# Optimization experiments

Measured on AMD Instinct MI355X. Metric: run time of the kernel, lower is better.

Reference implementation:

```python
import jax, jax.numpy as jnp
import numpy as np
import math

B, S, D, H = 4, 2048, 1024, 16
HD = D // H  # 64
SCALE = math.sqrt(HD)  # scale=True -> sqrt(d_model // n_head)

def setup_inputs() -> dict:
    key = jax.random.key(0)
    k1, k2, k3, k4, k5 = jax.random.split(key, 5)
    x = jax.random.normal(k1, (B, S, D), dtype=jnp.float32)
    char_ids = jax.random.randint(k2, (B, S), 0, 21128)
    seq_len = jax.random.randint(k3, (B,), 1, S)
    mask = jnp.ones((B, S), dtype=jnp.int64)
    W_qkv = jax.random.normal(k4, (D, 3 * D), dtype=jnp.float32) * (1.0 / math.sqrt(D))
    W_fc = jax.random.normal(k5, (D, D), dtype=jnp.float32) * (1.0 / math.sqrt(D))
    b_fc = jnp.zeros((D,), dtype=jnp.float32)
    return {"x": x, "char_ids": char_ids, "seq_len": seq_len, "mask": mask,
            "W_qkv": W_qkv, "W_fc": W_fc, "b_fc": b_fc}

def reference(x, char_ids, seq_len, mask, W_qkv, W_fc, b_fc):
    b, s, d = x.shape
    qkv = x @ W_qkv                      # [b, s, 3d]
    q, k, v = jnp.split(qkv, 3, axis=-1)
    # [b, h, s, hd]
    q = q.reshape(b, s, H, HD).transpose(0, 2, 1, 3)
    k = k.reshape(b, s, H, HD).transpose(0, 2, 1, 3)
    v = v.reshape(b, s, H, HD).transpose(0, 2, 1, 3)
    attn = jnp.einsum('bhqd,bhkd->bhqk', q, k) / SCALE
    attn = jnp.where(mask[:, None, None, :] == 0, -jnp.inf, attn)
    attn = jax.nn.softmax(attn, axis=-1)
    # dropout is identity in eval mode
    out = jnp.einsum('bhqk,bhkd->bhqd', attn, v)
    out = out.transpose(0, 2, 1, 3).reshape(b, s, d)
    return out @ W_fc + b_fc
```

## Files before the change

kernel.cpp:

```cpp
#include <hip/hip_runtime.h>
#include <hip/hip_bf16.h>


#define S_ 2048
#define D_ 1024

typedef __attribute__((ext_vector_type(4))) float f32x4;
typedef __attribute__((ext_vector_type(16))) float f32x16;
typedef __attribute__((ext_vector_type(8))) short bf16x8;

__device__ __forceinline__ unsigned short f2b(float f) {
  union { float f; unsigned u; } x; x.f = f;
  unsigned r = x.u + 0x7fffu + ((x.u >> 16) & 1u);
  return (unsigned short)(r >> 16);
}
__device__ __forceinline__ float b2f(unsigned short u) {
  union { unsigned u; float f; } x; x.u = ((unsigned)u) << 16; return x.f;
}

__device__ __forceinline__ void gload_lds16(const void* g, void* l) {
  __builtin_amdgcn_global_load_lds(
      (const __attribute__((address_space(1))) unsigned int*)g,
      (__attribute__((address_space(3))) unsigned int*)l, 16, 0, 0);
}

__global__ void cvt_f32_bf16(const float* __restrict__ in, unsigned short* __restrict__ out, int n) {
  int i = (blockIdx.x * blockDim.x + threadIdx.x) * 8;
  if (i >= n) return;
  float4 a = *(const float4*)&in[i];
  float4 b = *(const float4*)&in[i + 4];
  unsigned short r[8];
  r[0] = f2b(a.x); r[1] = f2b(a.y); r[2] = f2b(a.z); r[3] = f2b(a.w);
  r[4] = f2b(b.x); r[5] = f2b(b.y); r[6] = f2b(b.z); r[7] = f2b(b.w);
  *(uint4*)&out[i] = *(uint4*)r;
}

__global__ void transpose_cvt(const float* __restrict__ W, unsigned short* __restrict__ Wt,
                              int K, int N) {
  __shared__ unsigned short tile[32][33];
  int n0 = blockIdx.x * 32, k0 = blockIdx.y * 32;
  int tx = threadIdx.x & 31, ty = threadIdx.x >> 5;
  #pragma unroll
  for (int i = 0; i < 32; i += 8)
    tile[ty + i][tx] = f2b(W[(size_t)(k0 + ty + i) * N + n0 + tx]);
  __syncthreads();
  #pragma unroll
  for (int i = 0; i < 32; i += 8)
    Wt[(size_t)(n0 + ty + i) * K + k0 + tx] = tile[tx][ty + i];
}

__global__ __launch_bounds__(256) void gemm_bt(const unsigned short* __restrict__ A,
                                               const unsigned short* __restrict__ Bt,
                                               const float* __restrict__ bias,
                                               float* __restrict__ Cf,
                                               unsigned short* __restrict__ Cb,
                                               int M, int N, int K) {
  __shared__ unsigned short As[128 * 32];
  __shared__ unsigned short Bs[128 * 32];
  int tid = threadIdx.x, wave = tid >> 6, lane = tid & 63;
  int bm = blockIdx.x, bn = blockIdx.y;
  int wr = (wave >> 1) * 64, wc = (wave & 1) * 64;
  f32x4 acc[4][4] = {};

  const unsigned short* aG0 = A + (size_t)(bm * 128 + wave * 32 + (lane >> 2)) * K + (lane & 3) * 8;
  const unsigned short* aG1 = aG0 + (size_t)16 * K;
  const unsigned short* bG0 = Bt + (size_t)(bn * 128 + wave * 32 + (lane >> 2)) * K + (lane & 3) * 8;
  const unsigned short* bG1 = bG0 + (size_t)16 * K;
  unsigned short* aL0 = As + wave * 32 * 32;
  unsigned short* aL1 = aL0 + 16 * 32;
  unsigned short* bL0 = Bs + wave * 32 * 32;
  unsigned short* bL1 = bL0 + 16 * 32;

  for (int k0 = 0; k0 < K; k0 += 32) {
    gload_lds16(aG0, aL0); gload_lds16(aG1, aL1);
    gload_lds16(bG0, bL0); gload_lds16(bG1, bL1);
    aG0 += 32; aG1 += 32; bG0 += 32; bG1 += 32;
    __syncthreads();
    bf16x8 af[4], bf[4];
    #pragma unroll
    for (int i = 0; i < 4; i++)
      af[i] = *(const bf16x8*)&As[(wr + i * 16 + (lane & 15)) * 32 + (lane >> 4) * 8];
    #pragma unroll
    for (int i = 0; i < 4; i++)
      bf[i] = *(const bf16x8*)&Bs[(wc + i * 16 + (lane & 15)) * 32 + (lane >> 4) * 8];
    #pragma unroll
    for (int i = 0; i < 4; i++)
      #pragma unroll
      for (int j = 0; j < 4; j++)
        acc[i][j] = __builtin_amdgcn_mfma_f32_16x16x32_bf16(af[i], bf[j], acc[i][j], 0, 0, 0);
    __syncthreads();
  }

  int row0 = bm * 128 + wr + (lane >> 4) * 4;
  int col0 = bn * 128 + wc + (lane & 15);
  if (Cb) {
    #pragma unroll
    for (int i = 0; i < 4; i++)
      #pragma unroll
      for (int j = 0; j < 4; j++)
        #pragma unroll
        for (int q = 0; q < 4; q++)
          Cb[(size_t)(row0 + i * 16 + q) * N + col0 + j * 16] = f2b(acc[i][j][q]);
  } else {
    #pragma unroll
    for (int i = 0; i < 4; i++)
      #pragma unroll
      for (int j = 0; j < 4; j++) {
        float bv = bias[col0 + j * 16];
        #pragma unroll
        for (int q = 0; q < 4; q++)
          Cf[(size_t)(row0 + i * 16 + q) * N + col0 + j * 16] = acc[i][j][q] + bv;
      }
  }
}

__global__ __launch_bounds__(256) void flash_attn(const unsigned short* __restrict__ qkv,
                                                  unsigned short* __restrict__ ao) {
  __shared__ unsigned short Ks[2][4096];
  __shared__ unsigned short Vs[2][4096];
  int tid = threadIdx.x, wave = tid >> 6, lane = tid & 63;
  int l31 = lane & 31, hi = lane >> 5;
  int bh = blockIdx.x, b = bh >> 4, h = bh & 15;
  const unsigned short* base = qkv + (size_t)b * S_ * 3072 + h * 64;
  const unsigned short* kb = base + 1024;
  const unsigned short* vb = base + 2048;
  int q0 = blockIdx.y * 128 + wave * 32;

  bf16x8 qf[4];
  {
    const unsigned short* qp = base + (size_t)(q0 + l31) * 3072 + hi * 8;
    #pragma unroll
    for (int ks = 0; ks < 4; ks++) {
      bf16x8 v = *(const bf16x8*)(qp + ks * 16);
      #pragma unroll
      for (int e = 0; e < 8; e++) v[e] = (short)f2b(0.125f * b2f((unsigned short)v[e]));
      qf[ks] = v;
    }
  }

  f32x16 o0a = {}, o0b = {}, o1a = {}, o1b = {};
  float mi = -1e30f, li = 0.f;

  int r_l = lane >> 3;
  int gsrc = (lane & 7) ^ r_l;
  size_t koffA = (size_t)((wave * 2 + 0) * 8 + r_l) * 3072 + gsrc * 8;
  size_t koffB = (size_t)((wave * 2 + 1) * 8 + r_l) * 3072 + gsrc * 8;
  int kvv = tid & 63, dgr = (tid >> 6) * 16;
  bf16x8 vr0, vr1;

  {
    gload_lds16(kb + koffA, &Ks[0][(wave * 2 + 0) * 512]);
    gload_lds16(kb + koffB, &Ks[0][(wave * 2 + 1) * 512]);
    const unsigned short* vsrc = vb + (size_t)kvv * 3072 + dgr;
    vr0 = *(const bf16x8*)vsrc;
    vr1 = *(const bf16x8*)(vsrc + 8);
    #pragma unroll
    for (int e = 0; e < 16; e++) {
      int d = dgr + e;
      Vs[0][d * 64 + ((((kvv >> 3) ^ (d & 7)) << 3)) + (kvv & 7)] =
          (unsigned short)(e < 8 ? vr0[e] : vr1[e - 8]);
    }
    __syncthreads();
  }

  for (int t = 0; t < 32; ++t) {
    int cur = t & 1;
    int tn = (t + 1) & 31;
    {
      const unsigned short* ksrc = kb + (size_t)tn * 64 * 3072;
      gload_lds16(ksrc + koffA, &Ks[cur ^ 1][(wave * 2 + 0) * 512]);
      gload_lds16(ksrc + koffB, &Ks[cur ^ 1][(wave * 2 + 1) * 512]);
      const unsigned short* vsrc = vb + (size_t)(tn * 64 + kvv) * 3072 + dgr;
      vr0 = *(const bf16x8*)vsrc;
      vr1 = *(const bf16x8*)(vsrc + 8);
    }

    const unsigned short* Kc = Ks[cur];
    const unsigned short* Vc = Vs[cur];

    #pragma unroll
    for (int sub = 0; sub < 2; ++sub) {
      f32x16 sA = {};
      __builtin_amdgcn_s_setprio(1);
      #pragma unroll
      for (int ks = 0; ks < 4; ks++) {
        int row = sub * 32 + l31;
        bf16x8 kf = *(const bf16x8*)&Kc[row * 64 + ((((ks << 1) + hi) ^ (row & 7)) << 3)];
        sA = __builtin_amdgcn_mfma_f32_32x32x16_bf16(kf, qf[ks], sA, 0, 0, 0);
      }
      __builtin_amdgcn_s_setprio(0);

      float t0 = fmaxf(fmaxf(sA[0], sA[1]), sA[2]);
      float t1 = fmaxf(fmaxf(sA[3], sA[4]), sA[5]);
      float t2 = fmaxf(fmaxf(sA[6], sA[7]), sA[8]);
      float t3 = fmaxf(fmaxf(sA[9], sA[10]), sA[11]);
      float t4 = fmaxf(fmaxf(sA[12], sA[13]), sA[14]);
      float tm = fmaxf(fmaxf(fmaxf(t0, t1), t2), fmaxf(fmaxf(t3, t4), sA[15]));
      tm = fmaxf(tm, __shfl_xor(tm, 32, 64));
      if (__any(tm > mi + 8.f)) {
        float tnew = fmaxf(mi, tm);
        float fac = __expf(mi - tnew);
        li *= fac; mi = tnew;
        #pragma unroll
        for (int r = 0; r < 16; r++) {
          o0a[r] *= fac; o0b[r] *= fac; o1a[r] *= fac; o1b[r] *= fac;
        }
      }
      float p[16];
      float rs = 0.f;
      #pragma unroll
      for (int r = 0; r < 16; r++) { p[r] = __expf(sA[r] - mi); rs += p[r]; }
      li += rs;

      unsigned c0, c1, c2, c3, c4, c5, c6, c7;
      asm("v_cvt_pk_bf16_f32 %0, %1, %2" : "=v"(c0) : "v"(p[0]),  "v"(p[1]));
      asm("v_cvt_pk_bf16_f32 %0, %1, %2" : "=v"(c1) : "v"(p[2]),  "v"(p[3]));
      asm("v_cvt_pk_bf16_f32 %0, %1, %2" : "=v"(c2) : "v"(p[4]),  "v"(p[5]));
      asm("v_cvt_pk_bf16_f32 %0, %1, %2" : "=v"(c3) : "v"(p[6]),  "v"(p[7]));
      asm("v_cvt_pk_bf16_f32 %0, %1, %2" : "=v"(c4) : "v"(p[8]),  "v"(p[9]));
      asm("v_cvt_pk_bf16_f32 %0, %1, %2" : "=v"(c5) : "v"(p[10]), "v"(p[11]));
      asm("v_cvt_pk_bf16_f32 %0, %1, %2" : "=v"(c6) : "v"(p[12]), "v"(p[13]));
      asm("v_cvt_pk_bf16_f32 %0, %1, %2" : "=v"(c7) : "v"(p[14]), "v"(p[15]));
      asm volatile("v_permlane32_swap_b32 %0, %1" : "+v"(c0), "+v"(c2));
      asm volatile("v_permlane32_swap_b32 %0, %1" : "+v"(c1), "+v"(c3));
      asm volatile("v_permlane32_swap_b32 %0, %1" : "+v"(c4), "+v"(c6));
      asm volatile("v_permlane32_swap_b32 %0, %1" : "+v"(c5), "+v"(c7));
      union { unsigned u[4]; bf16x8 v; } P0, P1;
      P0.u[0] = c0; P0.u[1] = c1; P0.u[2] = c2; P0.u[3] = c3;
      P1.u[0] = c4; P1.u[1] = c5; P1.u[2] = c6; P1.u[3] = c7;

      int slot0 = (sub << 2) + hi;
      int slot1 = (sub << 2) + 2 + hi;
      bf16x8 vA0 = *(const bf16x8*)&Vc[l31 * 64 + ((slot0 ^ (l31 & 7)) << 3)];
      bf16x8 vA1 = *(const bf16x8*)&Vc[(32 + l31) * 64 + ((slot0 ^ (l31 & 7)) << 3)];
      bf16x8 vB0 = *(const bf16x8*)&Vc[l31 * 64 + ((slot1 ^ (l31 & 7)) << 3)];
      bf16x8 vB1 = *(const bf16x8*)&Vc[(32 + l31) * 64 + ((slot1 ^ (l31 & 7)) << 3)];
      __builtin_amdgcn_s_setprio(1);
      o0a = __builtin_amdgcn_mfma_f32_32x32x16_bf16(vA0, P0.v, o0a, 0, 0, 0);
      o1a = __builtin_amdgcn_mfma_f32_32x32x16_bf16(vA1, P0.v, o1a, 0, 0, 0);
      o0b = __builtin_amdgcn_mfma_f32_32x32x16_bf16(vB0, P1.v, o0b, 0, 0, 0);
      o1b = __builtin_amdgcn_mfma_f32_32x32x16_bf16(vB1, P1.v, o1b, 0, 0, 0);
      __builtin_amdgcn_s_setprio(0);
    }

    {
      unsigned short* Vd = Vs[cur ^ 1];
      #pragma unroll
      for (int e = 0; e < 16; e++) {
        int d = dgr + e;
        Vd[d * 64 + ((((kvv >> 3) ^ (d & 7)) << 3)) + (kvv & 7)] =
            (unsigned short)(e < 8 ? vr0[e] : vr1[e - 8]);
      }
    }
    __syncthreads();
  }

  li += __shfl_xor(li, 32, 64);
  float inv = 1.f / li;
  unsigned short* aop = ao + (size_t)(b * S_ + q0 + l31) * D_ + h * 64;
  #pragma unroll
  for (int g = 0; g < 4; g++) {
    union { unsigned short s[4]; uint2 u; } w0, w1;
    #pragma unroll
    for (int e = 0; e < 4; e++) {
      w0.s[e] = f2b((o0a[g * 4 + e] + o0b[g * 4 + e]) * inv);
      w1.s[e] = f2b((o1a[g * 4 + e] + o1b[g * 4 + e]) * inv);
    }
    int d = g * 8 + hi * 4;
    *(uint2*)&aop[d] = w0.u;
    *(uint2*)&aop[32 + d] = w1.u;
  }
}

extern "C" void kernel_launch(void* const* d_in, const int* in_sizes, int n_in,
                              void* d_out, int out_size, void* d_ws, size_t ws_size,
                              hipStream_t stream) {
  const float* x    = (const float*)d_in[0];
  const float* Wqkv = (const float*)d_in[4];
  const float* Wfc  = (const float*)d_in[5];
  const float* bfc  = (const float*)d_in[6];
  float* out = (float*)d_out;

  char* ws = (char*)d_ws;
  unsigned short* xb    = (unsigned short*)(ws);
  unsigned short* qkv   = (unsigned short*)(ws + 16777216);
  unsigned short* ao    = (unsigned short*)(ws + 67108864);
  unsigned short* wqkvT = (unsigned short*)(ws + 83886080);
  unsigned short* wfcT  = (unsigned short*)(ws + 90177536);

  cvt_f32_bf16<<<dim3(4096), dim3(256), 0, stream>>>(x, xb, 8388608);
  transpose_cvt<<<dim3(96, 32), dim3(256), 0, stream>>>(Wqkv, wqkvT, 1024, 3072);
  transpose_cvt<<<dim3(32, 32), dim3(256), 0, stream>>>(Wfc, wfcT, 1024, 1024);
  gemm_bt<<<dim3(64, 24), dim3(256), 0, stream>>>(xb, wqkvT, nullptr, nullptr, qkv, 8192, 3072, 1024);
  flash_attn<<<dim3(64, 16), dim3(256), 0, stream>>>(qkv, ao);
  gemm_bt<<<dim3(64, 8), dim3(256), 0, stream>>>(ao, wfcT, bfc, out, nullptr, 8192, 1024, 1024);
}
```

Before: 237.3 us.

## Fuse x fp32-to-bf16 conversion into QKV GEMM and swizzle workgroup order

Removes the standalone kernel that converted x to bf16. The QKV GEMM now loads fp32 x directly, converts it in registers and writes the result to LDS, which saves one launch and a 16MB write plus re-read. It also remaps workgroup indices in groups of 8 to improve L2 reuse of B tiles. The trade-off is that the fp32 A loads are synchronous register loads instead of async global-to-LDS loads. Since A is re-read once per N-tile (24 times), the fp32 read traffic for A doubles inside the GEMM.

```diff
diff --git a/kernel.cpp b/kernel.cpp
--- a/kernel.cpp
+++ b/kernel.cpp
@@ -22,17 +22,6 @@
   __builtin_amdgcn_global_load_lds(
       (const __attribute__((address_space(1))) unsigned int*)g,
       (__attribute__((address_space(3))) unsigned int*)l, 16, 0, 0);
-}
-
-__global__ void cvt_f32_bf16(const float* __restrict__ in, unsigned short* __restrict__ out, int n) {
-  int i = (blockIdx.x * blockDim.x + threadIdx.x) * 8;
-  if (i >= n) return;
-  float4 a = *(const float4*)&in[i];
-  float4 b = *(const float4*)&in[i + 4];
-  unsigned short r[8];
-  r[0] = f2b(a.x); r[1] = f2b(a.y); r[2] = f2b(a.z); r[3] = f2b(a.w);
-  r[4] = f2b(b.x); r[5] = f2b(b.y); r[6] = f2b(b.z); r[7] = f2b(b.w);
-  *(uint4*)&out[i] = *(uint4*)r;
 }
 
 __global__ void transpose_cvt(const float* __restrict__ W, unsigned short* __restrict__ Wt,
@@ -49,7 +38,8 @@
     Wt[(size_t)(n0 + ty + i) * K + k0 + tx] = tile[tx][ty + i];
 }
 
-__global__ __launch_bounds__(256) void gemm_bt(const unsigned short* __restrict__ A,
+template <bool AF32>
+__global__ __launch_bounds__(256) void gemm_bt(const void* __restrict__ Av,
                                                const unsigned short* __restrict__ Bt,
                                                const float* __restrict__ bias,
                                                float* __restrict__ Cf,
@@ -58,23 +48,49 @@
   __shared__ unsigned short As[128 * 32];
   __shared__ unsigned short Bs[128 * 32];
   int tid = threadIdx.x, wave = tid >> 6, lane = tid & 63;
-  int bm = blockIdx.x, bn = blockIdx.y;
+
+  int lin = blockIdx.y * 64 + blockIdx.x;
+  int nwg = gridDim.y * 64;
+  int qq = nwg >> 3;
+  int swz = (lin & 7) * qq + (lin >> 3);
+  int bm = swz & 63, bn = swz >> 6;
+
   int wr = (wave >> 1) * 64, wc = (wave & 1) * 64;
   f32x4 acc[4][4] = {};
 
-  const unsigned short* aG0 = A + (size_t)(bm * 128 + wave * 32 + (lane >> 2)) * K + (lane & 3) * 8;
-  const unsigned short* aG1 = aG0 + (size_t)16 * K;
-  const unsigned short* bG0 = Bt + (size_t)(bn * 128 + wave * 32 + (lane >> 2)) * K + (lane & 3) * 8;
+  int arow = wave * 32 + (lane >> 2);
+  int acol = (lane & 3) * 8;
+  const unsigned short* bG0 = Bt + (size_t)(bn * 128 + wave * 32 + (lane >> 2)) * K + acol;
   const unsigned short* bG1 = bG0 + (size_t)16 * K;
-  unsigned short* aL0 = As + wave * 32 * 32;
-  unsigned short* aL1 = aL0 + 16 * 32;
   unsigned short* bL0 = Bs + wave * 32 * 32;
   unsigned short* bL1 = bL0 + 16 * 32;
+  unsigned short* aW = As + arow * 32 + acol;
+
+  const unsigned short* aB16 = nullptr;
+  const float* aF32 = nullptr;
+  if constexpr (AF32) aF32 = (const float*)Av + (size_t)(bm * 128 + arow) * K + acol;
+  else                aB16 = (const unsigned short*)Av + (size_t)(bm * 128 + arow) * K + acol;
 
   for (int k0 = 0; k0 < K; k0 += 32) {
-    gload_lds16(aG0, aL0); gload_lds16(aG1, aL1);
     gload_lds16(bG0, bL0); gload_lds16(bG1, bL1);
-    aG0 += 32; aG1 += 32; bG0 += 32; bG1 += 32;
+    bG0 += 32; bG1 += 32;
+    if constexpr (AF32) {
+      float4 a0 = *(const float4*)aF32;
+      float4 a1 = *(const float4*)(aF32 + 4);
+      float4 c0 = *(const float4*)(aF32 + (size_t)16 * K);
+      float4 c1 = *(const float4*)(aF32 + (size_t)16 * K + 4);
+      aF32 += 32;
+      unsigned short r[8], s[8];
+      r[0]=f2b(a0.x); r[1]=f2b(a0.y); r[2]=f2b(a0.z); r[3]=f2b(a0.w);
+      r[4]=f2b(a1.x); r[5]=f2b(a1.y); r[6]=f2b(a1.z); r[7]=f2b(a1.w);
+      s[0]=f2b(c0.x); s[1]=f2b(c0.y); s[2]=f2b(c0.z); s[3]=f2b(c0.w);
+      s[4]=f2b(c1.x); s[5]=f2b(c1.y); s[6]=f2b(c1.z); s[7]=f2b(c1.w);
+      *(uint4*)aW = *(uint4*)r;
+      *(uint4*)(aW + 16 * 32) = *(uint4*)s;
+    } else {
+      gload_lds16(aB16, aW); gload_lds16(aB16 + (size_t)16 * K, aW + 16 * 32);
+      aB16 += 32;
+    }
     __syncthreads();
     bf16x8 af[4], bf[4];
     #pragma unroll
@@ -282,16 +298,16 @@
   float* out = (float*)d_out;
 
   char* ws = (char*)d_ws;
-  unsigned short* xb    = (unsigned short*)(ws);
-  unsigned short* qkv   = (unsigned short*)(ws + 16777216);
-  unsigned short* ao    = (unsigned short*)(ws + 67108864);
-  unsigned short* wqkvT = (unsigned short*)(ws + 83886080);
-  unsigned short* wfcT  = (unsigned short*)(ws + 90177536);
-
-  cvt_f32_bf16<<<dim3(4096), dim3(256), 0, stream>>>(x, xb, 8388608);
+  unsigned short* qkv   = (unsigned short*)(ws);
+  unsigned short* ao    = (unsigned short*)(ws + 50331648);
+  unsigned short* wqkvT = (unsigned short*)(ws + 67108864);
+  unsigned short* wfcT  = (unsigned short*)(ws + 73400320);
+
   transpose_cvt<<<dim3(96, 32), dim3(256), 0, stream>>>(Wqkv, wqkvT, 1024, 3072);
   transpose_cvt<<<dim3(32, 32), dim3(256), 0, stream>>>(Wfc, wfcT, 1024, 1024);
-  gemm_bt<<<dim3(64, 24), dim3(256), 0, stream>>>(xb, wqkvT, nullptr, nullptr, qkv, 8192, 3072, 1024);
+  gemm_bt<true><<<dim3(64, 24), dim3(256), 0, stream>>>(x, wqkvT, nullptr, nullptr, qkv,
+                                                        8192, 3072, 1024);
   flash_attn<<<dim3(64, 16), dim3(256), 0, stream>>>(qkv, ao);
-  gemm_bt<<<dim3(64, 8), dim3(256), 0, stream>>>(ao, wfcT, bfc, out, nullptr, 8192, 1024, 1024);
-}
+  gemm_bt<false><<<dim3(64, 8), dim3(256), 0, stream>>>(ao, wfcT, bfc, out, nullptr,
+                                                        8192, 1024, 1024);
+}
```

New measurement: 270.8 us. 14.1% more time.

## Process two query tiles per wave in flash attention to reuse K/V tiles

Applied to the files above, without the earlier changes.

Each wave now handles two 32-row query blocks (A and B, 128 rows apart), so each block covers 256 queries and the grid halves along y. The K and V fragments read from LDS and the global K/V loads are shared by twice as many query rows, cutting LDS and global traffic per unit of compute and adding independent MFMA chains for latency hiding. The cost is roughly double the accumulator and softmax register use, which may lower occupancy, and only 512 blocks are launched, which lowers parallelism on a large GPU.

```diff
diff --git a/kernel.cpp b/kernel.cpp
--- a/kernel.cpp
+++ b/kernel.cpp
@@ -124,22 +124,27 @@
   const unsigned short* base = qkv + (size_t)b * S_ * 3072 + h * 64;
   const unsigned short* kb = base + 1024;
   const unsigned short* vb = base + 2048;
-  int q0 = blockIdx.y * 128 + wave * 32;
-
-  bf16x8 qf[4];
+  int q0 = blockIdx.y * 256 + wave * 32;
+
+  bf16x8 qfA[4], qfB[4];
   {
-    const unsigned short* qp = base + (size_t)(q0 + l31) * 3072 + hi * 8;
+    const unsigned short* qpA = base + (size_t)(q0 + l31) * 3072 + hi * 8;
+    const unsigned short* qpB = qpA + (size_t)128 * 3072;
     #pragma unroll
     for (int ks = 0; ks < 4; ks++) {
-      bf16x8 v = *(const bf16x8*)(qp + ks * 16);
-      #pragma unroll
-      for (int e = 0; e < 8; e++) v[e] = (short)f2b(0.125f * b2f((unsigned short)v[e]));
-      qf[ks] = v;
-    }
-  }
-
-  f32x16 o0a = {}, o0b = {}, o1a = {}, o1b = {};
-  float mi = -1e30f, li = 0.f;
+      bf16x8 va = *(const bf16x8*)(qpA + ks * 16);
+      bf16x8 vc = *(const bf16x8*)(qpB + ks * 16);
+      #pragma unroll
+      for (int e = 0; e < 8; e++) {
+        va[e] = (short)f2b(0.125f * b2f((unsigned short)va[e]));
+        vc[e] = (short)f2b(0.125f * b2f((unsigned short)vc[e]));
+      }
+      qfA[ks] = va; qfB[ks] = vc;
+    }
+  }
+
+  f32x16 oA0 = {}, oA1 = {}, oB0 = {}, oB1 = {};
+  float miA = -1e30f, liA = 0.f, miB = -1e30f, liB = 0.f;
 
   int r_l = lane >> 3;
   int gsrc = (lane & 7) ^ r_l;
@@ -180,66 +185,107 @@
 
     #pragma unroll
     for (int sub = 0; sub < 2; ++sub) {
-      f32x16 sA = {};
+      f32x16 sA = {}, sB = {};
       __builtin_amdgcn_s_setprio(1);
       #pragma unroll
       for (int ks = 0; ks < 4; ks++) {
         int row = sub * 32 + l31;
         bf16x8 kf = *(const bf16x8*)&Kc[row * 64 + ((((ks << 1) + hi) ^ (row & 7)) << 3)];
-        sA = __builtin_amdgcn_mfma_f32_32x32x16_bf16(kf, qf[ks], sA, 0, 0, 0);
+        sA = __builtin_amdgcn_mfma_f32_32x32x16_bf16(kf, qfA[ks], sA, 0, 0, 0);
+        sB = __builtin_amdgcn_mfma_f32_32x32x16_bf16(kf, qfB[ks], sB, 0, 0, 0);
       }
       __builtin_amdgcn_s_setprio(0);
 
-      float t0 = fmaxf(fmaxf(sA[0], sA[1]), sA[2]);
-      float t1 = fmaxf(fmaxf(sA[3], sA[4]), sA[5]);
-      float t2 = fmaxf(fmaxf(sA[6], sA[7]), sA[8]);
-      float t3 = fmaxf(fmaxf(sA[9], sA[10]), sA[11]);
-      float t4 = fmaxf(fmaxf(sA[12], sA[13]), sA[14]);
-      float tm = fmaxf(fmaxf(fmaxf(t0, t1), t2), fmaxf(fmaxf(t3, t4), sA[15]));
-      tm = fmaxf(tm, __shfl_xor(tm, 32, 64));
-      if (__any(tm > mi + 8.f)) {
-        float tnew = fmaxf(mi, tm);
-        float fac = __expf(mi - tnew);
-        li *= fac; mi = tnew;
+      union { unsigned u[4]; bf16x8 v; } PA0, PA1;
+      {
+        float t0 = fmaxf(fmaxf(sA[0], sA[1]), sA[2]);
+        float t1 = fmaxf(fmaxf(sA[3], sA[4]), sA[5]);
+        float t2 = fmaxf(fmaxf(sA[6], sA[7]), sA[8]);
+        float t3 = fmaxf(fmaxf(sA[9], sA[10]), sA[11]);
+        float t4 = fmaxf(fmaxf(sA[12], sA[13]), sA[14]);
+        float tm = fmaxf(fmaxf(fmaxf(t0, t1), t2), fmaxf(fmaxf(t3, t4), sA[15]));
+        tm = fmaxf(tm, __shfl_xor(tm, 32, 64));
+        if (__any(tm > miA + 8.f)) {
+          float tnew = fmaxf(miA, tm);
+          float fac = __expf(miA - tnew);
+          liA *= fac; miA = tnew;
+          #pragma unroll
+          for (int r = 0; r < 16; r++) { oA0[r] *= fac; oA1[r] *= fac; }
+        }
+        float p[16];
+        float rs = 0.f;
         #pragma unroll
-        for (int r = 0; r < 16; r++) {
-          o0a[r] *= fac; o0b[r] *= fac; o1a[r] *= fac; o1b[r] *= fac;
+        for (int r = 0; r < 16; r++) { p[r] = __expf(sA[r] - miA); rs += p[r]; }
+        liA += rs;
+        unsigned c0, c1, c2, c3, c4, c5, c6, c7;
+        asm("v_cvt_pk_bf16_f32 %0, %1, %2" : "=v"(c0) : "v"(p[0]),  "v"(p[1]));
+        asm("v_cvt_pk_bf16_f32 %0, %1, %2" : "=v"(c1) : "v"(p[2]),  "v"(p[3]));
+        asm("v_cvt_pk_bf16_f32 %0, %1, %2" : "=v"(c2) : "v"(p[4]),  "v"(p[5]));
+        asm("v_cvt_pk_bf16_f32 %0, %1, %2" : "=v"(c3) : "v"(p[6]),  "v"(p[7]));
+        asm("v_cvt_pk_bf16_f32 %0, %1, %2" : "=v"(c4) : "v"(p[8]),  "v"(p[9]));
+        asm("v_cvt_pk_bf16_f32 %0, %1, %2" : "=v"(c5) : "v"(p[10]), "v"(p[11]));
+        asm("v_cvt_pk_bf16_f32 %0, %1, %2" : "=v"(c6) : "v"(p[12]), "v"(p[13]));
+        asm("v_cvt_pk_bf16_f32 %0, %1, %2" : "=v"(c7) : "v"(p[14]), "v"(p[15]));
+        asm volatile("v_permlane32_swap_b32 %0, %1" : "+v"(c0), "+v"(c2));
+        asm volatile("v_permlane32_swap_b32 %0, %1" : "+v"(c1), "+v"(c3));
+        asm volatile("v_permlane32_swap_b32 %0, %1" : "+v"(c4), "+v"(c6));
+        asm volatile("v_permlane32_swap_b32 %0, %1" : "+v"(c5), "+v"(c7));
+        PA0.u[0] = c0; PA0.u[1] = c1; PA0.u[2] = c2; PA0.u[3] = c3;
+        PA1.u[0] = c4; PA1.u[1] = c5; PA1.u[2] = c6; PA1.u[3] = c7;
+      }
+      union { unsigned u[4]; bf16x8 v; } PB0, PB1;
+      {
+        float t0 = fmaxf(fmaxf(sB[0], sB[1]), sB[2]);
+        float t1 = fmaxf(fmaxf(sB[3], sB[4]), sB[5]);
+        float t2 = fmaxf(fmaxf(sB[6], sB[7]), sB[8]);
+        float t3 = fmaxf(fmaxf(sB[9], sB[10]), sB[11]);
+        float t4 = fmaxf(fmaxf(sB[12], sB[13]), sB[14]);
+        float tm = fmaxf(fmaxf(fmaxf(t0, t1), t2), fmaxf(fmaxf(t3, t4), sB[15]));
+        tm = fmaxf(tm, __shfl_xor(tm, 32, 64));
+        if (__any(tm > miB + 8.f)) {
+          float tnew = fmaxf(miB, tm);
+          float fac = __expf(miB - tnew);
+          liB *= fac; miB = tnew;
+          #pragma unroll
+          for (int r = 0; r < 16; r++) { oB0[r] *= fac; oB1[r] *= fac; }
         }
-      }
-      float p[16];
-      float rs = 0.f;
-      #pragma unroll
-      for (int r = 0; r < 16; r++) { p[r] = __expf(sA[r] - mi); rs += p[r]; }
-      li += rs;
-
-      unsigned c0, c1, c2, c3, c4, c5, c6, c7;
-      asm("v_cvt_pk_bf16_f32 %0, %1, %2" : "=v"(c0) : "v"(p[0]),  "v"(p[1]));
-      asm("v_cvt_pk_bf16_f32 %0, %1, %2" : "=v"(c1) : "v"(p[2]),  "v"(p[3]));
-      asm("v_cvt_pk_bf16_f32 %0, %1, %2" : "=v"(c2) : "v"(p[4]),  "v"(p[5]));
-      asm("v_cvt_pk_bf16_f32 %0, %1, %2" : "=v"(c3) : "v"(p[6]),  "v"(p[7]));
-      asm("v_cvt_pk_bf16_f32 %0, %1, %2" : "=v"(c4) : "v"(p[8]),  "v"(p[9]));
-      asm("v_cvt_pk_bf16_f32 %0, %1, %2" : "=v"(c5) : "v"(p[10]), "v"(p[11]));
-      asm("v_cvt_pk_bf16_f32 %0, %1, %2" : "=v"(c6) : "v"(p[12]), "v"(p[13]));
-      asm("v_cvt_pk_bf16_f32 %0, %1, %2" : "=v"(c7) : "v"(p[14]), "v"(p[15]));
-      asm volatile("v_permlane32_swap_b32 %0, %1" : "+v"(c0), "+v"(c2));
-      asm volatile("v_permlane32_swap_b32 %0, %1" : "+v"(c1), "+v"(c3));
-      asm volatile("v_permlane32_swap_b32 %0, %1" : "+v"(c4), "+v"(c6));
-      asm volatile("v_permlane32_swap_b32 %0, %1" : "+v"(c5), "+v"(c7));
-      union { unsigned u[4]; bf16x8 v; } P0, P1;
-      P0.u[0] = c0; P0.u[1] = c1; P0.u[2] = c2; P0.u[3] = c3;
-      P1.u[0] = c4; P1.u[1] = c5; P1.u[2] = c6; P1.u[3] = c7;
+        float p[16];
+        float rs = 0.f;
+        #pragma unroll
+        for (int r = 0; r < 16; r++) { p[r] = __expf(sB[r] - miB); rs += p[r]; }
+        liB += rs;
+        unsigned c0, c1, c2, c3, c4, c5, c6, c7;
+        asm("v_cvt_pk_bf16_f32 %0, %1, %2" : "=v"(c0) : "v"(p[0]),  "v"(p[1]));
+        asm("v_cvt_pk_bf16_f32 %0, %1, %2" : "=v"(c1) : "v"(p[2]),  "v"(p[3]));
+        asm("v_cvt_pk_bf16_f32 %0, %1, %2" : "=v"(c2) : "v"(p[4]),  "v"(p[5]));
+        asm("v_cvt_pk_bf16_f32 %0, %1, %2" : "=v"(c3) : "v"(p[6]),  "v"(p[7]));
+        asm("v_cvt_pk_bf16_f32 %0, %1, %2" : "=v"(c4) : "v"(p[8]),  "v"(p[9]));
+        asm("v_cvt_pk_bf16_f32 %0, %1, %2" : "=v"(c5) : "v"(p[10]), "v"(p[11]));
+        asm("v_cvt_pk_bf16_f32 %0, %1, %2" : "=v"(c6) : "v"(p[12]), "v"(p[13]));
+        asm("v_cvt_pk_bf16_f32 %0, %1, %2" : "=v"(c7) : "v"(p[14]), "v"(p[15]));
+        asm volatile("v_permlane32_swap_b32 %0, %1" : "+v"(c0), "+v"(c2));
+        asm volatile("v_permlane32_swap_b32 %0, %1" : "+v"(c1), "+v"(c3));
+        asm volatile("v_permlane32_swap_b32 %0, %1" : "+v"(c4), "+v"(c6));
+        asm volatile("v_permlane32_swap_b32 %0, %1" : "+v"(c5), "+v"(c7));
+        PB0.u[0] = c0; PB0.u[1] = c1; PB0.u[2] = c2; PB0.u[3] = c3;
+        PB1.u[0] = c4; PB1.u[1] = c5; PB1.u[2] = c6; PB1.u[3] = c7;
+      }
 
       int slot0 = (sub << 2) + hi;
       int slot1 = (sub << 2) + 2 + hi;
-      bf16x8 vA0 = *(const bf16x8*)&Vc[l31 * 64 + ((slot0 ^ (l31 & 7)) << 3)];
-      bf16x8 vA1 = *(const bf16x8*)&Vc[(32 + l31) * 64 + ((slot0 ^ (l31 & 7)) << 3)];
-      bf16x8 vB0 = *(const bf16x8*)&Vc[l31 * 64 + ((slot1 ^ (l31 & 7)) << 3)];
-      bf16x8 vB1 = *(const bf16x8*)&Vc[(32 + l31) * 64 + ((slot1 ^ (l31 & 7)) << 3)];
+      bf16x8 v00 = *(const bf16x8*)&Vc[l31 * 64 + ((slot0 ^ (l31 & 7)) << 3)];
+      bf16x8 v01 = *(const bf16x8*)&Vc[(32 + l31) * 64 + ((slot0 ^ (l31 & 7)) << 3)];
+      bf16x8 v10 = *(const bf16x8*)&Vc[l31 * 64 + ((slot1 ^ (l31 & 7)) << 3)];
+      bf16x8 v11 = *(const bf16x8*)&Vc[(32 + l31) * 64 + ((slot1 ^ (l31 & 7)) << 3)];
       __builtin_amdgcn_s_setprio(1);
-      o0a = __builtin_amdgcn_mfma_f32_32x32x16_bf16(vA0, P0.v, o0a, 0, 0, 0);
-      o1a = __builtin_amdgcn_mfma_f32_32x32x16_bf16(vA1, P0.v, o1a, 0, 0, 0);
-      o0b = __builtin_amdgcn_mfma_f32_32x32x16_bf16(vB0, P1.v, o0b, 0, 0, 0);
-      o1b = __builtin_amdgcn_mfma_f32_32x32x16_bf16(vB1, P1.v, o1b, 0, 0, 0);
+      oA0 = __builtin_amdgcn_mfma_f32_32x32x16_bf16(v00, PA0.v, oA0, 0, 0, 0);
+      oB0 = __builtin_amdgcn_mfma_f32_32x32x16_bf16(v00, PB0.v, oB0, 0, 0, 0);
+      oA1 = __builtin_amdgcn_mfma_f32_32x32x16_bf16(v01, PA0.v, oA1, 0, 0, 0);
+      oB1 = __builtin_amdgcn_mfma_f32_32x32x16_bf16(v01, PB0.v, oB1, 0, 0, 0);
+      oA0 = __builtin_amdgcn_mfma_f32_32x32x16_bf16(v10, PA1.v, oA0, 0, 0, 0);
+      oB0 = __builtin_amdgcn_mfma_f32_32x32x16_bf16(v10, PB1.v, oB0, 0, 0, 0);
+      oA1 = __builtin_amdgcn_mfma_f32_32x32x16_bf16(v11, PA1.v, oA1, 0, 0, 0);
+      oB1 = __builtin_amdgcn_mfma_f32_32x32x16_bf16(v11, PB1.v, oB1, 0, 0, 0);
       __builtin_amdgcn_s_setprio(0);
     }
 
@@ -255,20 +301,26 @@
     __syncthreads();
   }
 
-  li += __shfl_xor(li, 32, 64);
-  float inv = 1.f / li;
-  unsigned short* aop = ao + (size_t)(b * S_ + q0 + l31) * D_ + h * 64;
+  liA += __shfl_xor(liA, 32, 64);
+  liB += __shfl_xor(liB, 32, 64);
+  float invA = 1.f / liA, invB = 1.f / liB;
+  unsigned short* aopA = ao + (size_t)(b * S_ + q0 + l31) * D_ + h * 64;
+  unsigned short* aopB = aopA + (size_t)128 * D_;
   #pragma unroll
   for (int g = 0; g < 4; g++) {
-    union { unsigned short s[4]; uint2 u; } w0, w1;
+    union { unsigned short s[4]; uint2 u; } wa0, wa1, wb0, wb1;
     #pragma unroll
     for (int e = 0; e < 4; e++) {
-      w0.s[e] = f2b((o0a[g * 4 + e] + o0b[g * 4 + e]) * inv);
-      w1.s[e] = f2b((o1a[g * 4 + e] + o1b[g * 4 + e]) * inv);
+      wa0.s[e] = f2b(oA0[g * 4 + e] * invA);
+      wa1.s[e] = f2b(oA1[g * 4 + e] * invA);
+      wb0.s[e] = f2b(oB0[g * 4 + e] * invB);
+      wb1.s[e] = f2b(oB1[g * 4 + e] * invB);
     }
     int d = g * 8 + hi * 4;
-    *(uint2*)&aop[d] = w0.u;
-    *(uint2*)&aop[32 + d] = w1.u;
+    *(uint2*)&aopA[d] = wa0.u;
+    *(uint2*)&aopA[32 + d] = wa1.u;
+    *(uint2*)&aopB[d] = wb0.u;
+    *(uint2*)&aopB[32 + d] = wb1.u;
   }
 }
 
@@ -292,6 +344,6 @@
   transpose_cvt<<<dim3(96, 32), dim3(256), 0, stream>>>(Wqkv, wqkvT, 1024, 3072);
   transpose_cvt<<<dim3(32, 32), dim3(256), 0, stream>>>(Wfc, wfcT, 1024, 1024);
   gemm_bt<<<dim3(64, 24), dim3(256), 0, stream>>>(xb, wqkvT, nullptr, nullptr, qkv, 8192, 3072, 1024);
-  flash_attn<<<dim3(64, 16), dim3(256), 0, stream>>>(qkv, ao);
+  flash_attn<<<dim3(64, 8), dim3(256), 0, stream>>>(qkv, ao);
   gemm_bt<<<dim3(64, 8), dim3(256), 0, stream>>>(ao, wfcT, bfc, out, nullptr, 8192, 1024, 1024);
 }
```

New measurement: 221.7 us. -6.5%, faster.

## Split flash attention KV range across two wave groups and merge partial softmax

Applied to the files above, without the earlier changes.

The flash attention block grows to 512 threads. Two 4-wave halves each process half of the key/value sequence for the same 128 queries, then combine their partial outputs through shared memory using the running max and sum statistics. V tile staging is also reworked to write packed 32-bit pairs into LDS instead of 16 scalar stores. The output accumulators are merged into two registers per wave instead of four. This is meant to raise wave-level parallelism and occupancy and to cut LDS store count, at the cost of a shared-memory reduction step, a larger LDS footprint, and a longer dependent MFMA chain.

```diff
diff --git a/kernel.cpp b/kernel.cpp
--- a/kernel.cpp
+++ b/kernel.cpp
@@ -114,17 +114,20 @@
   }
 }
 
-__global__ __launch_bounds__(256) void flash_attn(const unsigned short* __restrict__ qkv,
-                                                  unsigned short* __restrict__ ao) {
-  __shared__ unsigned short Ks[2][4096];
-  __shared__ unsigned short Vs[2][4096];
+__global__ __launch_bounds__(512, 4) void flash_attn(const unsigned short* __restrict__ qkv,
+                                                     unsigned short* __restrict__ ao) {
+  __shared__ unsigned short Ks[2][2][4096];
+  __shared__ unsigned short Vs[2][2][4096];
+  __shared__ float mstat[4][32][2];
   int tid = threadIdx.x, wave = tid >> 6, lane = tid & 63;
+  int half = wave >> 2, w4 = wave & 3;
+  int tid256 = tid & 255;
   int l31 = lane & 31, hi = lane >> 5;
   int bh = blockIdx.x, b = bh >> 4, h = bh & 15;
   const unsigned short* base = qkv + (size_t)b * S_ * 3072 + h * 64;
-  const unsigned short* kb = base + 1024;
-  const unsigned short* vb = base + 2048;
-  int q0 = blockIdx.y * 128 + wave * 32;
+  const unsigned short* kb = base + 1024 + (size_t)(half * 16) * 64 * 3072;
+  const unsigned short* vb = base + 2048 + (size_t)(half * 16) * 64 * 3072;
+  int q0 = blockIdx.y * 128 + w4 * 32;
 
   bf16x8 qf[4];
   {
@@ -138,45 +141,51 @@
     }
   }
 
-  f32x16 o0a = {}, o0b = {}, o1a = {}, o1b = {};
+  f32x16 o0 = {}, o1 = {};
   float mi = -1e30f, li = 0.f;
 
   int r_l = lane >> 3;
   int gsrc = (lane & 7) ^ r_l;
-  size_t koffA = (size_t)((wave * 2 + 0) * 8 + r_l) * 3072 + gsrc * 8;
-  size_t koffB = (size_t)((wave * 2 + 1) * 8 + r_l) * 3072 + gsrc * 8;
-  int kvv = tid & 63, dgr = (tid >> 6) * 16;
+  size_t koffA = (size_t)((w4 * 2 + 0) * 8 + r_l) * 3072 + gsrc * 8;
+  size_t koffB = (size_t)((w4 * 2 + 1) * 8 + r_l) * 3072 + gsrc * 8;
+  int kvp = (tid256 & 31) * 2, dgr = (tid256 >> 5) * 8;
+  int vslot = kvp >> 3;
+  int vlo = kvp & 7;
   bf16x8 vr0, vr1;
 
   {
-    gload_lds16(kb + koffA, &Ks[0][(wave * 2 + 0) * 512]);
-    gload_lds16(kb + koffB, &Ks[0][(wave * 2 + 1) * 512]);
-    const unsigned short* vsrc = vb + (size_t)kvv * 3072 + dgr;
+    gload_lds16(kb + koffA, &Ks[half][0][(w4 * 2 + 0) * 512]);
+    gload_lds16(kb + koffB, &Ks[half][0][(w4 * 2 + 1) * 512]);
+    const unsigned short* vsrc = vb + (size_t)kvp * 3072 + dgr;
     vr0 = *(const bf16x8*)vsrc;
-    vr1 = *(const bf16x8*)(vsrc + 8);
-    #pragma unroll
-    for (int e = 0; e < 16; e++) {
-      int d = dgr + e;
-      Vs[0][d * 64 + ((((kvv >> 3) ^ (d & 7)) << 3)) + (kvv & 7)] =
-          (unsigned short)(e < 8 ? vr0[e] : vr1[e - 8]);
+    vr1 = *(const bf16x8*)(vsrc + 3072);
+    union { bf16x8 v; unsigned u[4]; } a0, a1;
+    a0.v = vr0; a1.v = vr1;
+    #pragma unroll
+    for (int i = 0; i < 4; i++) {
+      int d0 = dgr + 2 * i, d1 = d0 + 1;
+      unsigned we = (a0.u[i] & 0xffffu) | (a1.u[i] << 16);
+      unsigned wo = (a0.u[i] >> 16) | (a1.u[i] & 0xffff0000u);
+      *(unsigned*)&Vs[half][0][d0 * 64 + ((vslot ^ (d0 & 7)) << 3) + vlo] = we;
+      *(unsigned*)&Vs[half][0][d1 * 64 + ((vslot ^ (d1 & 7)) << 3) + vlo] = wo;
     }
     __syncthreads();
   }
 
-  for (int t = 0; t < 32; ++t) {
-    int cur = t & 1;
-    int tn = (t + 1) & 31;
-    {
+  for (int tt = 0; tt < 16; ++tt) {
+    int cur = tt & 1;
+    if (tt < 15) {
+      int tn = tt + 1;
       const unsigned short* ksrc = kb + (size_t)tn * 64 * 3072;
-      gload_lds16(ksrc + koffA, &Ks[cur ^ 1][(wave * 2 + 0) * 512]);
-      gload_lds16(ksrc + koffB, &Ks[cur ^ 1][(wave * 2 + 1) * 512]);
-      const unsigned short* vsrc = vb + (size_t)(tn * 64 + kvv) * 3072 + dgr;
+      gload_lds16(ksrc + koffA, &Ks[half][cur ^ 1][(w4 * 2 + 0) * 512]);
+      gload_lds16(ksrc + koffB, &Ks[half][cur ^ 1][(w4 * 2 + 1) * 512]);
+      const unsigned short* vsrc = vb + (size_t)(tn * 64 + kvp) * 3072 + dgr;
       vr0 = *(const bf16x8*)vsrc;
-      vr1 = *(const bf16x8*)(vsrc + 8);
-    }
-
-    const unsigned short* Kc = Ks[cur];
-    const unsigned short* Vc = Vs[cur];
+      vr1 = *(const bf16x8*)(vsrc + 3072);
+    }
+
+    const unsigned short* Kc = Ks[half][cur];
+    const unsigned short* Vc = Vs[half][cur];
 
     #pragma unroll
     for (int sub = 0; sub < 2; ++sub) {
@@ -202,9 +211,7 @@
         float fac = __expf(mi - tnew);
         li *= fac; mi = tnew;
         #pragma unroll
-        for (int r = 0; r < 16; r++) {
-          o0a[r] *= fac; o0b[r] *= fac; o1a[r] *= fac; o1b[r] *= fac;
-        }
+        for (int r = 0; r < 16; r++) { o0[r] *= fac; o1[r] *= fac; }
       }
       float p[16];
       float rs = 0.f;
@@ -231,44 +238,66 @@
 
       int slot0 = (sub << 2) + hi;
       int slot1 = (sub << 2) + 2 + hi;
-      bf16x8 vA0 = *(const bf16x8*)&Vc[l31 * 64 + ((slot0 ^ (l31 & 7)) << 3)];
-      bf16x8 vA1 = *(const bf16x8*)&Vc[(32 + l31) * 64 + ((slot0 ^ (l31 & 7)) << 3)];
-      bf16x8 vB0 = *(const bf16x8*)&Vc[l31 * 64 + ((slot1 ^ (l31 & 7)) << 3)];
-      bf16x8 vB1 = *(const bf16x8*)&Vc[(32 + l31) * 64 + ((slot1 ^ (l31 & 7)) << 3)];
+      bf16x8 v00 = *(const bf16x8*)&Vc[l31 * 64 + ((slot0 ^ (l31 & 7)) << 3)];
+      bf16x8 v01 = *(const bf16x8*)&Vc[(32 + l31) * 64 + ((slot0 ^ (l31 & 7)) << 3)];
+      bf16x8 v10 = *(const bf16x8*)&Vc[l31 * 64 + ((slot1 ^ (l31 & 7)) << 3)];
+      bf16x8 v11 = *(const bf16x8*)&Vc[(32 + l31) * 64 + ((slot1 ^ (l31 & 7)) << 3)];
       __builtin_amdgcn_s_setprio(1);
-      o0a = __builtin_amdgcn_mfma_f32_32x32x16_bf16(vA0, P0.v, o0a, 0, 0, 0);
-      o1a = __builtin_amdgcn_mfma_f32_32x32x16_bf16(vA1, P0.v, o1a, 0, 0, 0);
-      o0b = __builtin_amdgcn_mfma_f32_32x32x16_bf16(vB0, P1.v, o0b, 0, 0, 0);
-      o1b = __builtin_amdgcn_mfma_f32_32x32x16_bf16(vB1, P1.v, o1b, 0, 0, 0);
+      o0 = __builtin_amdgcn_mfma_f32_32x32x16_bf16(v00, P0.v, o0, 0, 0, 0);
+      o1 = __builtin_amdgcn_mfma_f32_32x32x16_bf16(v01, P0.v, o1, 0, 0, 0);
+      o0 = __builtin_amdgcn_mfma_f32_32x32x16_bf16(v10, P1.v, o0, 0, 0, 0);
+      o1 = __builtin_amdgcn_mfma_f32_32x32x16_bf16(v11, P1.v, o1, 0, 0, 0);
       __builtin_amdgcn_s_setprio(0);
     }
 
-    {
-      unsigned short* Vd = Vs[cur ^ 1];
-      #pragma unroll
-      for (int e = 0; e < 16; e++) {
-        int d = dgr + e;
-        Vd[d * 64 + ((((kvv >> 3) ^ (d & 7)) << 3)) + (kvv & 7)] =
-            (unsigned short)(e < 8 ? vr0[e] : vr1[e - 8]);
+    if (tt < 15) {
+      unsigned short* Vd = Vs[half][cur ^ 1];
+      union { bf16x8 v; unsigned u[4]; } a0, a1;
+      a0.v = vr0; a1.v = vr1;
+      #pragma unroll
+      for (int i = 0; i < 4; i++) {
+        int d0 = dgr + 2 * i, d1 = d0 + 1;
+        unsigned we = (a0.u[i] & 0xffffu) | (a1.u[i] << 16);
+        unsigned wo = (a0.u[i] >> 16) | (a1.u[i] & 0xffff0000u);
+        *(unsigned*)&Vd[d0 * 64 + ((vslot ^ (d0 & 7)) << 3) + vlo] = we;
+        *(unsigned*)&Vd[d1 * 64 + ((vslot ^ (d1 & 7)) << 3) + vlo] = wo;
       }
     }
     __syncthreads();
   }
 
   li += __shfl_xor(li, 32, 64);
-  float inv = 1.f / li;
-  unsigned short* aop = ao + (size_t)(b * S_ + q0 + l31) * D_ + h * 64;
-  #pragma unroll
-  for (int g = 0; g < 4; g++) {
-    union { unsigned short s[4]; uint2 u; } w0, w1;
-    #pragma unroll
-    for (int e = 0; e < 4; e++) {
-      w0.s[e] = f2b((o0a[g * 4 + e] + o0b[g * 4 + e]) * inv);
-      w1.s[e] = f2b((o1a[g * 4 + e] + o1b[g * 4 + e]) * inv);
-    }
-    int d = g * 8 + hi * 4;
-    *(uint2*)&aop[d] = w0.u;
-    *(uint2*)&aop[32 + d] = w1.u;
+
+  float* obuf = (float*)&Ks[0][0][0];
+  if (half == 1) {
+    if (lane < 32) { mstat[w4][l31][0] = mi; mstat[w4][l31][1] = li; }
+    int idx = (w4 * 64 + lane) * 32;
+    #pragma unroll
+    for (int j = 0; j < 16; j++) { obuf[idx + j] = o0[j]; obuf[idx + 16 + j] = o1[j]; }
+  }
+  __syncthreads();
+
+  if (half == 0) {
+    float m1 = mstat[w4][l31][0], l1 = mstat[w4][l31][1];
+    float m = fmaxf(mi, m1);
+    float f0 = __expf(mi - m), f1 = __expf(m1 - m);
+    float inv = 1.f / (li * f0 + l1 * f1);
+    float g0 = f0 * inv, g1 = f1 * inv;
+    int idx = (w4 * 64 + lane) * 32;
+    unsigned short* aop = ao + (size_t)(b * S_ + q0 + l31) * D_ + h * 64;
+    #pragma unroll
+    for (int g = 0; g < 4; g++) {
+      union { unsigned short s[4]; uint2 u; } w0, w1;
+      #pragma unroll
+      for (int e = 0; e < 4; e++) {
+        int j = g * 4 + e;
+        w0.s[e] = f2b(o0[j] * g0 + obuf[idx + j] * g1);
+        w1.s[e] = f2b(o1[j] * g0 + obuf[idx + 16 + j] * g1);
+      }
+      int d = g * 8 + hi * 4;
+      *(uint2*)&aop[d] = w0.u;
+      *(uint2*)&aop[32 + d] = w1.u;
+    }
   }
 }
 
@@ -292,6 +321,6 @@
   transpose_cvt<<<dim3(96, 32), dim3(256), 0, stream>>>(Wqkv, wqkvT, 1024, 3072);
   transpose_cvt<<<dim3(32, 32), dim3(256), 0, stream>>>(Wfc, wfcT, 1024, 1024);
   gemm_bt<<<dim3(64, 24), dim3(256), 0, stream>>>(xb, wqkvT, nullptr, nullptr, qkv, 8192, 3072, 1024);
-  flash_attn<<<dim3(64, 16), dim3(256), 0, stream>>>(qkv, ao);
+  flash_attn<<<dim3(64, 16), dim3(512), 0, stream>>>(qkv, ao);
   gemm_bt<<<dim3(64, 8), dim3(256), 0, stream>>>(ao, wfcT, bfc, out, nullptr, 8192, 1024, 1024);
 }
```

Result: faster. 228.8 us (-3.6%).
